# Kernel optimization log

Measured on AMD Instinct MI355X. Metric: run time of the kernel, lower is better.

The kernel has to match this reference:

```python
import jax, jax.numpy as jnp
import numpy as np

N = 50000
E = 800000
IN = 256
C = 64  # hidden_channels
H = 4   # heads
NEG_SLOPE = 0.2


def _rand(key, shape, scale=0.05):
    return jax.random.normal(key, shape, dtype=jnp.float32) * scale


def setup_inputs() -> dict:
    key = jax.random.key(0)
    ks = jax.random.split(key, 32)
    inp = {
        'x': jax.random.normal(ks[0], (N, IN), dtype=jnp.float32),
        'edge_index': jax.random.randint(ks[1], (2, E), 0, N, dtype=jnp.int64),
        'edge_attr': jax.random.uniform(ks[2], (E, 1), dtype=jnp.float32),
    }
    ki = 3
    for l, din in zip((1, 2, 3), (IN, C, C)):
        inp[f'Wl{l}'] = _rand(ks[ki + 0], (din, H * C))
        inp[f'bl{l}'] = jnp.zeros((H * C,), jnp.float32)
        inp[f'Wr{l}'] = _rand(ks[ki + 1], (din, H * C))
        inp[f'br{l}'] = jnp.zeros((H * C,), jnp.float32)
        inp[f'We{l}'] = _rand(ks[ki + 2], (1, H * C))
        inp[f'att{l}'] = _rand(ks[ki + 3], (H, C))
        inp[f'bias{l}'] = jnp.zeros((C,), jnp.float32)
        ki += 4
    inp['prelu_w'] = jnp.full((C,), 0.25, jnp.float32)  # nn.PReLU default init
    return inp


def gatv2_layer(x, src, dst, eattr, Wl, bl, Wr, br, We, att, bias, n):
    h, c = att.shape
    xl = (x @ Wl + bl).reshape(n, h, c)   # source transform
    xr = (x @ Wr + br).reshape(n, h, c)   # destination transform
    ee = (eattr @ We).reshape(-1, h, c)   # edge-feature transform
    m = xl[src] + xr[dst] + ee            # [E', H, C] per-edge messages
    score = jnp.sum(jax.nn.leaky_relu(m, NEG_SLOPE) * att, axis=-1)  # [E', H]
    # segment softmax over destination node neighborhoods (PyG softmax, eps=1e-16)
    mx = jax.ops.segment_max(score, dst, num_segments=n)
    mx = jnp.where(jnp.isfinite(mx), mx, 0.0)
    ex = jnp.exp(score - mx[dst])
    den = jax.ops.segment_sum(ex, dst, num_segments=n)
    alpha = ex / (den[dst] + 1e-16)
    out = jax.ops.segment_sum(alpha[:, :, None] * xl[src], dst, num_segments=n)
    return out.mean(axis=1) + bias        # concat=False -> head mean, then bias


def reference(x, edge_index, edge_attr,
              Wl1, bl1, Wr1, br1, We1, att1, bias1,
              Wl2, bl2, Wr2, br2, We2, att2, bias2,
              Wl3, bl3, Wr3, br3, We3, att3, bias3,
              prelu_w):
    src, dst = edge_index[0], edge_index[1]
    n = x.shape[0]
    # add_self_loops with fill_value='mean': self-loop attr = mean of incoming edge_attr
    cnt = jax.ops.segment_sum(jnp.ones((src.shape[0],), jnp.float32), dst, num_segments=n)
    loop_attr = jax.ops.segment_sum(edge_attr, dst, num_segments=n) / jnp.maximum(cnt, 1.0)[:, None]
    loops = jnp.arange(n, dtype=src.dtype)
    src2 = jnp.concatenate([src, loops])
    dst2 = jnp.concatenate([dst, loops])
    ea2 = jnp.concatenate([edge_attr, loop_attr], axis=0)

    h = gatv2_layer(x, src2, dst2, ea2, Wl1, bl1, Wr1, br1, We1, att1, bias1, n)
    h = gatv2_layer(h, src2, dst2, ea2, Wl2, bl2, Wr2, br2, We2, att2, bias2, n)
    h = gatv2_layer(h, src2, dst2, ea2, Wl3, bl3, Wr3, br3, We3, att3, bias3, n)
    return jnp.where(h >= 0, h, prelu_w * h)  # PReLU per-channel
```

## Files before the change

kernel.cpp:

```cpp
#include <hip/hip_runtime.h>

#define HC 256
#define CCH 64
#define NEG 0.2f

__device__ __forceinline__ float lk(float m) { return m > 0.f ? m : NEG * m; }


__global__ void deg_kernel(const int* __restrict__ dst,
                           const float* __restrict__ eattr,
                           int* __restrict__ cnt, float* __restrict__ sumf, int E) {
  int e = blockIdx.x * blockDim.x + threadIdx.x;
  if (e >= E) return;
  int d = dst[e];
  atomicAdd(&cnt[d], 1);
  atomicAdd(&sumf[d], eattr[e]);
}

__global__ __launch_bounds__(1024)
void scanA(const int* __restrict__ cnt, const float* __restrict__ sumf,
           int* __restrict__ rowptr, float* __restrict__ loopat,
           int* __restrict__ btot, int n) {
  __shared__ int wsum[16];
  int tid = threadIdx.x, lane = tid & 63, w = tid >> 6;
  int i = blockIdx.x * 1024 + tid;
  int v = (i < n) ? cnt[i] : 0;
  int s = v;
  #pragma unroll
  for (int off = 1; off < 64; off <<= 1) {
    int t = __shfl_up(s, off, 64);
    if (lane >= off) s += t;
  }
  if (lane == 63) wsum[w] = s;
  __syncthreads();
  int woff = 0;
  for (int j = 0; j < w; j++) woff += wsum[j];
  if (i < n) {
    rowptr[i] = woff + s - v;
    loopat[i] = sumf[i] / fmaxf((float)v, 1.0f);
  }
  if (tid == 1023) btot[blockIdx.x] = woff + s;
}

__global__ void scanB(const int* __restrict__ btot, int* __restrict__ boff,
                      int* __restrict__ rowptr_n, int nb) {
  int lane = threadIdx.x;
  int v = (lane < nb) ? btot[lane] : 0;
  int s = v;
  #pragma unroll
  for (int off = 1; off < 64; off <<= 1) {
    int t = __shfl_up(s, off, 64);
    if (lane >= off) s += t;
  }
  if (lane < nb) boff[lane] = s - v;
  if (lane == 63) *rowptr_n = s;
}

__global__ void scanC(int* __restrict__ rowptr, const int* __restrict__ boff, int n) {
  int i = blockIdx.x * blockDim.x + threadIdx.x;
  if (i < n) rowptr[i] += boff[i >> 10];
}

__global__ void csr_fill_kernel(const int* __restrict__ src,
                                const int* __restrict__ dst,
                                const float* __restrict__ eattr,
                                const int* __restrict__ rowptr,
                                int* __restrict__ fill,
                                int* __restrict__ csr_src, float* __restrict__ csr_ea, int E) {
  int e = blockIdx.x * blockDim.x + threadIdx.x;
  if (e >= E) return;
  int d = dst[e];
  int p = atomicAdd(&fill[d], 1);
  int slot = rowptr[d] + p;
  csr_src[slot] = src[e];
  csr_ea[slot] = eattr[e];
}


__device__ __forceinline__ void fma8(float a, const float4 blo, const float4 bhi,
                                     float4& c0, float4& c1) {
  c0.x = fmaf(a, blo.x, c0.x); c0.y = fmaf(a, blo.y, c0.y);
  c0.z = fmaf(a, blo.z, c0.z); c0.w = fmaf(a, blo.w, c0.w);
  c1.x = fmaf(a, bhi.x, c1.x); c1.y = fmaf(a, bhi.y, c1.y);
  c1.z = fmaf(a, bhi.z, c1.z); c1.w = fmaf(a, bhi.w, c1.w);
}

__global__ __launch_bounds__(256, 3)
void gemm128(const float* __restrict__ A,
             const float* __restrict__ Wl, const float* __restrict__ bl,
             const float* __restrict__ Wr, const float* __restrict__ br,
             float* __restrict__ xl, float* __restrict__ xr,
             int nrows, int K) {
  __shared__ float As[16][132];
  __shared__ float Ws[16][132];
  const float* W; const float* bb; float* out;
  if (blockIdx.x < 2) { W = Wl; bb = bl; out = xl; }
  else                { W = Wr; bb = br; out = xr; }
  int bn = (blockIdx.x & 1) * 128;
  int bm = blockIdx.y * 128;
  int tid = threadIdx.x;
  int tx = tid & 15, ty = tid >> 4;
  int arow = tid & 127;
  int akk  = (tid >> 7) * 8;
  int wkk  = tid >> 4;
  int wc   = (tid & 15) * 4;

  int row0 = bm + arow;
  bool aval = row0 < nrows;
  const float* arp = A + (size_t)row0 * K + akk;
  const float* wrp = W + (size_t)wkk * HC + bn + wc;

  float4 z = make_float4(0.f, 0.f, 0.f, 0.f);
  float4 a0 = aval ? *(const float4*)arp       : z;
  float4 a1 = aval ? *(const float4*)(arp + 4) : z;
  float4 w0 = *(const float4*)wrp;
  float4 w1 = *(const float4*)(wrp + 64);

  float4 c0[8], c1[8];
  #pragma unroll
  for (int i = 0; i < 8; i++) { c0[i] = z; c1[i] = z; }

  int k0 = 0;
  while (true) {
    As[akk+0][arow] = a0.x; As[akk+1][arow] = a0.y;
    As[akk+2][arow] = a0.z; As[akk+3][arow] = a0.w;
    As[akk+4][arow] = a1.x; As[akk+5][arow] = a1.y;
    As[akk+6][arow] = a1.z; As[akk+7][arow] = a1.w;
    *(float4*)&Ws[wkk][wc]      = w0;
    *(float4*)&Ws[wkk][wc + 64] = w1;
    __syncthreads();
    k0 += 16;
    bool more = k0 < K;
    if (more) {
      a0 = aval ? *(const float4*)(arp + k0)     : z;
      a1 = aval ? *(const float4*)(arp + k0 + 4) : z;
      w0 = *(const float4*)(wrp + (size_t)k0 * HC);
      w1 = *(const float4*)(wrp + (size_t)k0 * HC + 64);
    }
    #pragma unroll
    for (int k = 0; k < 16; k++) {
      float4 alo = *(const float4*)&As[k][ty * 8];
      float4 ahi = *(const float4*)&As[k][ty * 8 + 4];
      float4 blo = *(const float4*)&Ws[k][tx * 4];
      float4 bhi = *(const float4*)&Ws[k][tx * 4 + 64];
      fma8(alo.x, blo, bhi, c0[0], c1[0]);
      fma8(alo.y, blo, bhi, c0[1], c1[1]);
      fma8(alo.z, blo, bhi, c0[2], c1[2]);
      fma8(alo.w, blo, bhi, c0[3], c1[3]);
      fma8(ahi.x, blo, bhi, c0[4], c1[4]);
      fma8(ahi.y, blo, bhi, c0[5], c1[5]);
      fma8(ahi.z, blo, bhi, c0[6], c1[6]);
      fma8(ahi.w, blo, bhi, c0[7], c1[7]);
    }
    if (!more) break;
    __syncthreads();
  }

  float4 bv0 = *(const float4*)(bb + bn + tx * 4);
  float4 bv1 = *(const float4*)(bb + bn + tx * 4 + 64);
  #pragma unroll
  for (int i = 0; i < 8; i++) {
    int row = bm + ty * 8 + i;
    if (row < nrows) {
      float* op = out + (size_t)row * HC + bn + tx * 4;
      float4 o0, o1;
      o0.x = c0[i].x + bv0.x; o0.y = c0[i].y + bv0.y;
      o0.z = c0[i].z + bv0.z; o0.w = c0[i].w + bv0.w;
      o1.x = c1[i].x + bv1.x; o1.y = c1[i].y + bv1.y;
      o1.z = c1[i].z + bv1.z; o1.w = c1[i].w + bv1.w;
      *(float4*)op        = o0;
      *(float4*)(op + 64) = o1;
    }
  }
}


template<int B>
__device__ __forceinline__ void proc_edges(
    const float* __restrict__ xl, int i,
    const int* __restrict__ csr_src, const float* __restrict__ csr_ea,
    const float4 xr4, const float4 we4, const float4 ah4, int l4,
    float& mx, float& den, float4& acc) {
  int sn[B]; float ea[B]; float4 v[B]; float s[B];
  #pragma unroll
  for (int j = 0; j < B; j++) { sn[j] = csr_src[i + j]; ea[j] = csr_ea[i + j]; }
  #pragma unroll
  for (int j = 0; j < B; j++)
    v[j] = *(const float4*)(xl + (size_t)sn[j] * HC + l4);
  #pragma unroll
  for (int j = 0; j < B; j++) {
    float mx_ = fmaf(ea[j], we4.x, v[j].x + xr4.x);
    float my_ = fmaf(ea[j], we4.y, v[j].y + xr4.y);
    float mz_ = fmaf(ea[j], we4.z, v[j].z + xr4.z);
    float mw_ = fmaf(ea[j], we4.w, v[j].w + xr4.w);
    s[j] = lk(mx_) * ah4.x + lk(my_) * ah4.y + lk(mz_) * ah4.z + lk(mw_) * ah4.w;
  }
  #pragma unroll
  for (int off = 8; off >= 1; off >>= 1)
    #pragma unroll
    for (int j = 0; j < B; j++) s[j] += __shfl_xor(s[j], off, 64);
  float bm = s[0];
  #pragma unroll
  for (int j = 1; j < B; j++) bm = fmaxf(bm, s[j]);
  float newm = fmaxf(mx, bm);
  float r = __expf(mx - newm);
  den *= r; acc.x *= r; acc.y *= r; acc.z *= r; acc.w *= r;
  #pragma unroll
  for (int j = 0; j < B; j++) {
    float p = __expf(s[j] - newm);
    den += p;
    acc.x = fmaf(p, v[j].x, acc.x);
    acc.y = fmaf(p, v[j].y, acc.y);
    acc.z = fmaf(p, v[j].z, acc.z);
    acc.w = fmaf(p, v[j].w, acc.w);
  }
  mx = newm;
}

__global__ __launch_bounds__(256)
void gat_edge(const float* __restrict__ xl, const float* __restrict__ xr,
              const float* __restrict__ loopat, const int* __restrict__ rowptr,
              const int* __restrict__ csr_src, const float* __restrict__ csr_ea,
              const float* __restrict__ We, const float* __restrict__ att,
              const float* __restrict__ bias, const float* __restrict__ prelu_w,
              float* __restrict__ out, int n, int is_last) {
  int node = blockIdx.x;
  int l    = threadIdx.x & 63;
  int wv   = threadIdx.x >> 6;
  int l4   = l * 4;
  float4 we4 = *(const float4*)(We + l4);
  float4 ah4 = *(const float4*)(att + l4);
  float4 xr4 = *(const float4*)(xr + (size_t)node * HC + l4);

  float mx, den; float4 acc;
  if (wv == 0) {
    float4 vs = *(const float4*)(xl + (size_t)node * HC + l4);
    float la = loopat[node];
    float mx_ = fmaf(la, we4.x, vs.x + xr4.x);
    float my_ = fmaf(la, we4.y, vs.y + xr4.y);
    float mz_ = fmaf(la, we4.z, vs.z + xr4.z);
    float mw_ = fmaf(la, we4.w, vs.w + xr4.w);
    float t = lk(mx_) * ah4.x + lk(my_) * ah4.y + lk(mz_) * ah4.z + lk(mw_) * ah4.w;
    #pragma unroll
    for (int off = 8; off >= 1; off >>= 1) t += __shfl_xor(t, off, 64);
    mx = t; den = 1.f; acc = vs;
  } else {
    mx = -3.4e38f; den = 0.f; acc = make_float4(0.f, 0.f, 0.f, 0.f);
  }

  int beg = rowptr[node], end = rowptr[node + 1];
  int per = (end - beg + 3) >> 2;
  int wbeg = beg + wv * per;
  int wend = min(wbeg + per, end);
  int i = wbeg;
  for (; i + 4 <= wend; i += 4)
    proc_edges<4>(xl, i, csr_src, csr_ea, xr4, we4, ah4, l4, mx, den, acc);
  for (; i < wend; i++)
    proc_edges<1>(xl, i, csr_src, csr_ea, xr4, we4, ah4, l4, mx, den, acc);

  __shared__ float  s_mx[4][4];
  __shared__ float  s_den[4][4];
  __shared__ float4 s_acc[4][64];
  int h = l >> 4;
  s_acc[wv][l] = acc;
  if ((l & 15) == 0) { s_mx[wv][h] = mx; s_den[wv][h] = den; }
  __syncthreads();
  if (wv == 0) {
    float M = fmaxf(fmaxf(s_mx[0][h], s_mx[1][h]), fmaxf(s_mx[2][h], s_mx[3][h]));
    float dt = 0.f;
    float4 a = make_float4(0.f, 0.f, 0.f, 0.f);
    #pragma unroll
    for (int w = 0; w < 4; w++) {
      float f = __expf(s_mx[w][h] - M);
      dt = fmaf(s_den[w][h], f, dt);
      float4 aw = s_acc[w][l];
      a.x = fmaf(aw.x, f, a.x);
      a.y = fmaf(aw.y, f, a.y);
      a.z = fmaf(aw.z, f, a.z);
      a.w = fmaf(aw.w, f, a.w);
    }
    float inv = 1.f / (dt + 1e-16f);
    a.x *= inv; a.y *= inv; a.z *= inv; a.w *= inv;
    a.x += __shfl_xor(a.x, 16, 64); a.x += __shfl_xor(a.x, 32, 64);
    a.y += __shfl_xor(a.y, 16, 64); a.y += __shfl_xor(a.y, 32, 64);
    a.z += __shfl_xor(a.z, 16, 64); a.z += __shfl_xor(a.z, 32, 64);
    a.w += __shfl_xor(a.w, 16, 64); a.w += __shfl_xor(a.w, 32, 64);
    if (l < 16) {
      int c = l * 4;
      float4 bv = *(const float4*)(bias + c);
      float4 o;
      o.x = 0.25f * a.x + bv.x;
      o.y = 0.25f * a.y + bv.y;
      o.z = 0.25f * a.z + bv.z;
      o.w = 0.25f * a.w + bv.w;
      if (is_last) {
        float4 pw = *(const float4*)(prelu_w + c);
        o.x = o.x >= 0.f ? o.x : pw.x * o.x;
        o.y = o.y >= 0.f ? o.y : pw.y * o.y;
        o.z = o.z >= 0.f ? o.z : pw.z * o.z;
        o.w = o.w >= 0.f ? o.w : pw.w * o.w;
      }
      *(float4*)(out + (size_t)node * CCH + c) = o;
    }
  }
}


extern "C" void kernel_launch(void* const* d_in, const int* in_sizes, int n_in,
                              void* d_out, int out_size, void* d_ws, size_t ws_size,
                              hipStream_t stream) {
  const float* x     = (const float*)d_in[0];
  const int*   ei    = (const int*)d_in[1];
  const float* eattr = (const float*)d_in[2];
  int N = in_sizes[0] / HC;
  int E = in_sizes[1] / 2;
  const int* src = ei;
  const int* dst = ei + E;

  const float* Wl[3]  = {(const float*)d_in[3],  (const float*)d_in[10], (const float*)d_in[17]};
  const float* bl[3]  = {(const float*)d_in[4],  (const float*)d_in[11], (const float*)d_in[18]};
  const float* Wr[3]  = {(const float*)d_in[5],  (const float*)d_in[12], (const float*)d_in[19]};
  const float* br[3]  = {(const float*)d_in[6],  (const float*)d_in[13], (const float*)d_in[20]};
  const float* Wev[3] = {(const float*)d_in[7],  (const float*)d_in[14], (const float*)d_in[21]};
  const float* attv[3]= {(const float*)d_in[8],  (const float*)d_in[15], (const float*)d_in[22]};
  const float* bias[3]= {(const float*)d_in[9],  (const float*)d_in[16], (const float*)d_in[23]};
  const float* prelu  = (const float*)d_in[24];

  char* p = (char*)d_ws;
  float* xl     = (float*)p; p += (size_t)N * HC * 4;
  float* xr     = (float*)p; p += (size_t)N * HC * 4;
  float* hbuf   = (float*)p; p += (size_t)N * CCH * 4;
  int*   cnt    = (int*)p;   p += (size_t)N * 4;
  int*   fill   = (int*)p;   p += (size_t)N * 4;
  float* sumf   = (float*)p; p += (size_t)N * 4;
  float* loopat = (float*)p; p += (size_t)N * 4;
  int*   rowptr = (int*)p;   p += (size_t)(N + 8) * 4;
  int*   btot   = (int*)p;   p += 64 * 4;
  int*   boff   = (int*)p;   p += 64 * 4;
  int*   csr_src= (int*)p;   p += (size_t)E * 4;
  float* csr_ea = (float*)p; p += (size_t)E * 4;

  hipMemsetAsync(cnt, 0, (size_t)N * 3 * 4, stream);

  int tb = 256;
  int nb = (N + 1023) / 1024;
  deg_kernel<<<dim3((E + tb - 1) / tb), dim3(tb), 0, stream>>>(dst, eattr, cnt, sumf, E);
  scanA<<<dim3(nb), dim3(1024), 0, stream>>>(cnt, sumf, rowptr, loopat, btot, N);
  scanB<<<dim3(1), dim3(64), 0, stream>>>(btot, boff, rowptr + N, nb);
  scanC<<<dim3((N + tb - 1) / tb), dim3(tb), 0, stream>>>(rowptr, boff, N);
  csr_fill_kernel<<<dim3((E + tb - 1) / tb), dim3(tb), 0, stream>>>(src, dst, eattr, rowptr,
                                                                    fill, csr_src, csr_ea, E);

  const float* in = x;
  int K = 256;
  for (int l = 0; l < 3; l++) {
    dim3 g(4, (N + 127) / 128);
    gemm128<<<g, dim3(256), 0, stream>>>(in, Wl[l], bl[l], Wr[l], br[l], xl, xr, N, K);
    float* o = (l == 2) ? (float*)d_out : hbuf;
    gat_edge<<<dim3(N), dim3(256), 0, stream>>>(xl, xr, loopat, rowptr, csr_src, csr_ea,
                                                Wev[l], attv[l], bias[l], prelu, o, N, l == 2);
    in = hbuf;
    K = CCH;
  }
}
```

Baseline: 896.6 us.

## Assign one wavefront per node in GAT edge kernel and double-buffer GEMM tiles

The edge-aggregation kernel now processes one destination node per wavefront (four nodes per block) instead of splitting a node's edges across four wavefronts. This removes the shared-memory merge of partial softmax states and the block barrier, and adds an 8-edge unrolled path. Separately, the GEMM uses double-buffered shared-memory tiles so only one barrier is needed per k-step. The trade-off is less parallelism per node for high-degree nodes and more shared memory per GEMM block, which may lower occupancy.

New measurement: 3.313 ms. 3.7x slower.

```diff
diff --git a/kernel.cpp b/kernel.cpp
--- a/kernel.cpp
+++ b/kernel.cpp
@@ -91,8 +91,8 @@
              const float* __restrict__ Wr, const float* __restrict__ br,
              float* __restrict__ xl, float* __restrict__ xr,
              int nrows, int K) {
-  __shared__ float As[16][132];
-  __shared__ float Ws[16][132];
+  __shared__ float As[2][16][132];
+  __shared__ float Ws[2][16][132];
   const float* W; const float* bb; float* out;
   if (blockIdx.x < 2) { W = Wl; bb = bl; out = xl; }
   else                { W = Wr; bb = br; out = xr; }
@@ -116,33 +116,35 @@
   float4 w0 = *(const float4*)wrp;
   float4 w1 = *(const float4*)(wrp + 64);
 
+  As[0][akk+0][arow] = a0.x; As[0][akk+1][arow] = a0.y;
+  As[0][akk+2][arow] = a0.z; As[0][akk+3][arow] = a0.w;
+  As[0][akk+4][arow] = a1.x; As[0][akk+5][arow] = a1.y;
+  As[0][akk+6][arow] = a1.z; As[0][akk+7][arow] = a1.w;
+  *(float4*)&Ws[0][wkk][wc]      = w0;
+  *(float4*)&Ws[0][wkk][wc + 64] = w1;
+
   float4 c0[8], c1[8];
   #pragma unroll
   for (int i = 0; i < 8; i++) { c0[i] = z; c1[i] = z; }
 
-  int k0 = 0;
-  while (true) {
-    As[akk+0][arow] = a0.x; As[akk+1][arow] = a0.y;
-    As[akk+2][arow] = a0.z; As[akk+3][arow] = a0.w;
-    As[akk+4][arow] = a1.x; As[akk+5][arow] = a1.y;
-    As[akk+6][arow] = a1.z; As[akk+7][arow] = a1.w;
-    *(float4*)&Ws[wkk][wc]      = w0;
-    *(float4*)&Ws[wkk][wc + 64] = w1;
-    __syncthreads();
-    k0 += 16;
-    bool more = k0 < K;
+  int NT = K >> 4;
+  int cur = 0;
+  for (int t = 0; t < NT; t++) {
+    bool more = (t + 1) < NT;
     if (more) {
+      int k0 = (t + 1) << 4;
       a0 = aval ? *(const float4*)(arp + k0)     : z;
       a1 = aval ? *(const float4*)(arp + k0 + 4) : z;
       w0 = *(const float4*)(wrp + (size_t)k0 * HC);
       w1 = *(const float4*)(wrp + (size_t)k0 * HC + 64);
     }
+    __syncthreads();
     #pragma unroll
     for (int k = 0; k < 16; k++) {
-      float4 alo = *(const float4*)&As[k][ty * 8];
-      float4 ahi = *(const float4*)&As[k][ty * 8 + 4];
-      float4 blo = *(const float4*)&Ws[k][tx * 4];
-      float4 bhi = *(const float4*)&Ws[k][tx * 4 + 64];
+      float4 alo = *(const float4*)&As[cur][k][ty * 8];
+      float4 ahi = *(const float4*)&As[cur][k][ty * 8 + 4];
+      float4 blo = *(const float4*)&Ws[cur][k][tx * 4];
+      float4 bhi = *(const float4*)&Ws[cur][k][tx * 4 + 64];
       fma8(alo.x, blo, bhi, c0[0], c1[0]);
       fma8(alo.y, blo, bhi, c0[1], c1[1]);
       fma8(alo.z, blo, bhi, c0[2], c1[2]);
@@ -152,8 +154,16 @@
       fma8(ahi.z, blo, bhi, c0[6], c1[6]);
       fma8(ahi.w, blo, bhi, c0[7], c1[7]);
     }
-    if (!more) break;
-    __syncthreads();
+    if (more) {
+      int nb2 = cur ^ 1;
+      As[nb2][akk+0][arow] = a0.x; As[nb2][akk+1][arow] = a0.y;
+      As[nb2][akk+2][arow] = a0.z; As[nb2][akk+3][arow] = a0.w;
+      As[nb2][akk+4][arow] = a1.x; As[nb2][akk+5][arow] = a1.y;
+      As[nb2][akk+6][arow] = a1.z; As[nb2][akk+7][arow] = a1.w;
+      *(float4*)&Ws[nb2][wkk][wc]      = w0;
+      *(float4*)&Ws[nb2][wkk][wc + 64] = w1;
+      cur = nb2;
+    }
   }
 
   float4 bv0 = *(const float4*)(bb + bn + tx * 4);
@@ -224,84 +234,60 @@
               const float* __restrict__ We, const float* __restrict__ att,
               const float* __restrict__ bias, const float* __restrict__ prelu_w,
               float* __restrict__ out, int n, int is_last) {
-  int node = blockIdx.x;
-  int l    = threadIdx.x & 63;
   int wv   = threadIdx.x >> 6;
-  int l4   = l * 4;
+  int node = blockIdx.x * 4 + wv;
+  if (node >= n) return;
+  int l  = threadIdx.x & 63;
+  int l4 = l * 4;
   float4 we4 = *(const float4*)(We + l4);
   float4 ah4 = *(const float4*)(att + l4);
   float4 xr4 = *(const float4*)(xr + (size_t)node * HC + l4);
 
-  float mx, den; float4 acc;
-  if (wv == 0) {
-    float4 vs = *(const float4*)(xl + (size_t)node * HC + l4);
-    float la = loopat[node];
-    float mx_ = fmaf(la, we4.x, vs.x + xr4.x);
-    float my_ = fmaf(la, we4.y, vs.y + xr4.y);
-    float mz_ = fmaf(la, we4.z, vs.z + xr4.z);
-    float mw_ = fmaf(la, we4.w, vs.w + xr4.w);
-    float t = lk(mx_) * ah4.x + lk(my_) * ah4.y + lk(mz_) * ah4.z + lk(mw_) * ah4.w;
-    #pragma unroll
-    for (int off = 8; off >= 1; off >>= 1) t += __shfl_xor(t, off, 64);
-    mx = t; den = 1.f; acc = vs;
-  } else {
-    mx = -3.4e38f; den = 0.f; acc = make_float4(0.f, 0.f, 0.f, 0.f);
-  }
+  float4 vs = *(const float4*)(xl + (size_t)node * HC + l4);
+  float la = loopat[node];
+  float mx_ = fmaf(la, we4.x, vs.x + xr4.x);
+  float my_ = fmaf(la, we4.y, vs.y + xr4.y);
+  float mz_ = fmaf(la, we4.z, vs.z + xr4.z);
+  float mw_ = fmaf(la, we4.w, vs.w + xr4.w);
+  float t = lk(mx_) * ah4.x + lk(my_) * ah4.y + lk(mz_) * ah4.z + lk(mw_) * ah4.w;
+  #pragma unroll
+  for (int off = 8; off >= 1; off >>= 1) t += __shfl_xor(t, off, 64);
+  float mx = t, den = 1.f; float4 acc = vs;
 
   int beg = rowptr[node], end = rowptr[node + 1];
-  int per = (end - beg + 3) >> 2;
-  int wbeg = beg + wv * per;
-  int wend = min(wbeg + per, end);
-  int i = wbeg;
-  for (; i + 4 <= wend; i += 4)
+  int i = beg;
+  for (; i + 8 <= end; i += 8)
+    proc_edges<8>(xl, i, csr_src, csr_ea, xr4, we4, ah4, l4, mx, den, acc);
+  if (i + 4 <= end) {
     proc_edges<4>(xl, i, csr_src, csr_ea, xr4, we4, ah4, l4, mx, den, acc);
-  for (; i < wend; i++)
+    i += 4;
+  }
+  for (; i < end; i++)
     proc_edges<1>(xl, i, csr_src, csr_ea, xr4, we4, ah4, l4, mx, den, acc);
 
-  __shared__ float  s_mx[4][4];
-  __shared__ float  s_den[4][4];
-  __shared__ float4 s_acc[4][64];
-  int h = l >> 4;
-  s_acc[wv][l] = acc;
-  if ((l & 15) == 0) { s_mx[wv][h] = mx; s_den[wv][h] = den; }
-  __syncthreads();
-  if (wv == 0) {
-    float M = fmaxf(fmaxf(s_mx[0][h], s_mx[1][h]), fmaxf(s_mx[2][h], s_mx[3][h]));
-    float dt = 0.f;
-    float4 a = make_float4(0.f, 0.f, 0.f, 0.f);
-    #pragma unroll
-    for (int w = 0; w < 4; w++) {
-      float f = __expf(s_mx[w][h] - M);
-      dt = fmaf(s_den[w][h], f, dt);
-      float4 aw = s_acc[w][l];
-      a.x = fmaf(aw.x, f, a.x);
-      a.y = fmaf(aw.y, f, a.y);
-      a.z = fmaf(aw.z, f, a.z);
-      a.w = fmaf(aw.w, f, a.w);
-    }
-    float inv = 1.f / (dt + 1e-16f);
-    a.x *= inv; a.y *= inv; a.z *= inv; a.w *= inv;
-    a.x += __shfl_xor(a.x, 16, 64); a.x += __shfl_xor(a.x, 32, 64);
-    a.y += __shfl_xor(a.y, 16, 64); a.y += __shfl_xor(a.y, 32, 64);
-    a.z += __shfl_xor(a.z, 16, 64); a.z += __shfl_xor(a.z, 32, 64);
-    a.w += __shfl_xor(a.w, 16, 64); a.w += __shfl_xor(a.w, 32, 64);
-    if (l < 16) {
-      int c = l * 4;
-      float4 bv = *(const float4*)(bias + c);
-      float4 o;
-      o.x = 0.25f * a.x + bv.x;
-      o.y = 0.25f * a.y + bv.y;
-      o.z = 0.25f * a.z + bv.z;
-      o.w = 0.25f * a.w + bv.w;
-      if (is_last) {
-        float4 pw = *(const float4*)(prelu_w + c);
-        o.x = o.x >= 0.f ? o.x : pw.x * o.x;
-        o.y = o.y >= 0.f ? o.y : pw.y * o.y;
-        o.z = o.z >= 0.f ? o.z : pw.z * o.z;
-        o.w = o.w >= 0.f ? o.w : pw.w * o.w;
-      }
-      *(float4*)(out + (size_t)node * CCH + c) = o;
-    }
+  float inv = 1.f / (den + 1e-16f);
+  float4 a;
+  a.x = acc.x * inv; a.y = acc.y * inv; a.z = acc.z * inv; a.w = acc.w * inv;
+  a.x += __shfl_xor(a.x, 16, 64); a.x += __shfl_xor(a.x, 32, 64);
+  a.y += __shfl_xor(a.y, 16, 64); a.y += __shfl_xor(a.y, 32, 64);
+  a.z += __shfl_xor(a.z, 16, 64); a.z += __shfl_xor(a.z, 32, 64);
+  a.w += __shfl_xor(a.w, 16, 64); a.w += __shfl_xor(a.w, 32, 64);
+  if (l < 16) {
+    int c = l * 4;
+    float4 bv = *(const float4*)(bias + c);
+    float4 o;
+    o.x = 0.25f * a.x + bv.x;
+    o.y = 0.25f * a.y + bv.y;
+    o.z = 0.25f * a.z + bv.z;
+    o.w = 0.25f * a.w + bv.w;
+    if (is_last) {
+      float4 pw = *(const float4*)(prelu_w + c);
+      o.x = o.x >= 0.f ? o.x : pw.x * o.x;
+      o.y = o.y >= 0.f ? o.y : pw.y * o.y;
+      o.z = o.z >= 0.f ? o.z : pw.z * o.z;
+      o.w = o.w >= 0.f ? o.w : pw.w * o.w;
+    }
+    *(float4*)(out + (size_t)node * CCH + c) = o;
   }
 }
 
@@ -357,8 +343,10 @@
     dim3 g(4, (N + 127) / 128);
     gemm128<<<g, dim3(256), 0, stream>>>(in, Wl[l], bl[l], Wr[l], br[l], xl, xr, N, K);
     float* o = (l == 2) ? (float*)d_out : hbuf;
-    gat_edge<<<dim3(N), dim3(256), 0, stream>>>(xl, xr, loopat, rowptr, csr_src, csr_ea,
-                                                Wev[l], attv[l], bias[l], prelu, o, N, l == 2);
+    gat_edge<<<dim3((N + 3) / 4), dim3(256), 0, stream>>>(xl, xr, loopat, rowptr,
+                                                          csr_src, csr_ea,
+                                                          Wev[l], attv[l], bias[l], prelu,
+                                                          o, N, l == 2);
     in = hbuf;
     K = CCH;
   }
```
